# Performance work log

Hardware: AMD Instinct MI355X
Metric: run time of the kernel (lower is better)

## Reference

```python
import jax, jax.numpy as jnp
import numpy as np

N = 100000   # nodes
E = 625000   # edges
D = 128      # feature dim (layers = [128,128,128])
H = 8        # attention heads
HD = 16      # head dim (H*HD == D)


def setup_inputs() -> dict:
    key = jax.random.key(0)
    ks = jax.random.split(key, 16)
    s = 1.0 / np.sqrt(D).astype(np.float32)
    inp = {
        'x': jax.random.normal(ks[0], (N, D), dtype=jnp.float32),
        'edge_index': jax.random.randint(ks[1], (2, E), 0, N, dtype=jnp.int64),
        'W1': jax.random.normal(ks[2], (D, D), dtype=jnp.float32) * s,
        'b1': jnp.zeros((D,), jnp.float32),
        'W2': jax.random.normal(ks[3], (D, D), dtype=jnp.float32) * s,
        'b2': jnp.zeros((D,), jnp.float32),
        'Wq': jax.random.normal(ks[4], (D, H * HD), dtype=jnp.float32) * s,
        'bq': jnp.zeros((H * HD,), jnp.float32),
        'Wk': jax.random.normal(ks[5], (D, H * HD), dtype=jnp.float32) * s,
        'bk': jnp.zeros((H * HD,), jnp.float32),
        'Wv': jax.random.normal(ks[6], (D, H * HD), dtype=jnp.float32) * s,
        'bv': jnp.zeros((H * HD,), jnp.float32),
        'Wo': jax.random.normal(ks[7], (H * HD, D), dtype=jnp.float32) * s,
        'bo': jnp.zeros((D,), jnp.float32),
    }
    return inp


def _gcn_conv(x, W, b, src, dst):
    """PyG GCNConv: x' = D^-1/2 (A+I) D^-1/2 (x W) + b, symmetric norm with self-loops."""
    h = x @ W                                   # [N, Dout]
    # degree at targets, +1 for self-loop
    deg = jnp.ones((N,), h.dtype).at[dst].add(jnp.ones((E,), h.dtype))
    dinv = jax.lax.rsqrt(deg)                   # [N]
    norm = dinv[src] * dinv[dst]                # [E]
    agg = jnp.zeros_like(h).at[dst].add(h[src] * norm[:, None])
    agg = agg + h * (dinv * dinv)[:, None]      # self-loop term
    return agg + b


def _mha_seq1(x, Wq, bq, Wk, bk, Wv, bv, Wo, bo):
    """Faithful to the hand-rolled MHA: batch=N, implied seq_len=1."""
    n = x.shape[0]
    q = (x @ Wq + bq).reshape(n, 1, H, HD).transpose(0, 2, 1, 3)  # [N,H,1,HD]
    k = (x @ Wk + bk).reshape(n, 1, H, HD).transpose(0, 2, 1, 3)
    v = (x @ Wv + bv).reshape(n, 1, H, HD).transpose(0, 2, 1, 3)
    scores = jnp.einsum('nhqd,nhkd->nhqk', q, k) / np.float32(np.sqrt(HD))
    attn = jax.nn.softmax(scores, axis=-1)                        # [N,H,1,1]
    out = jnp.einsum('nhqk,nhkd->nhqd', attn, v)                  # [N,H,1,HD]
    out = out.transpose(0, 2, 1, 3).reshape(n, 1, H * HD)
    return out @ Wo + bo                                          # [N,1,D]


def reference(x, edge_index, W1, b1, W2, b2, Wq, bq, Wk, bk, Wv, bv, Wo, bo):
    src, dst = edge_index[0], edge_index[1]
    h = _gcn_conv(x, W1, b1, src, dst)
    h = jax.nn.relu(h)                 # dropout is identity in eval
    h = _gcn_conv(h, W2, b2, src, dst) # last conv: no relu
    return _mha_seq1(h, Wq, bq, Wk, bk, Wv, bv, Wo, bo)
```

## Files before the change

kernel.cpp:

```cpp
#include <hip/hip_runtime.h>
#include <hip/hip_bf16.h>

#define DD 128
#define CAP 16
#define OVF_MAX 8192
#define ECHUNK 2048

typedef __bf16 bf16x8v __attribute__((ext_vector_type(8)));
typedef float  f32x4   __attribute__((ext_vector_type(4)));

__device__ inline unsigned short f2bf(float f) {
    unsigned u = __builtin_bit_cast(unsigned, f);
    unsigned r = (u + 0x7fffu + ((u >> 16) & 1u)) >> 16;
    return (unsigned short)r;
}
__device__ inline float bflo2f(unsigned p) { return __builtin_bit_cast(float, p << 16); }
__device__ inline float bfhi2f(unsigned p) { return __builtin_bit_cast(float, p & 0xffff0000u); }
__device__ inline float rl_f(int v, int i) {
    return __builtin_bit_cast(float, __builtin_amdgcn_readlane(v, i));
}

__global__ __launch_bounds__(256) void k_zero(int* __restrict__ a, int N) {
    int i = blockIdx.x * 256 + threadIdx.x;
    int stride = gridDim.x * 256;
    for (; i <= N; i += stride) a[i] = 0;
}

__global__ __launch_bounds__(256) void k_fill_fuse1(const int* __restrict__ src, const int* __restrict__ dst,
                                                    int* __restrict__ fillc, int* __restrict__ srcp,
                                                    int* __restrict__ ovfcnt, int2* __restrict__ ovf,
                                                    int E, int N, int FB,
                                                    const float* __restrict__ Wv, const float* __restrict__ Wo,
                                                    const float* __restrict__ bv, const float* __restrict__ bo,
                                                    float* __restrict__ Wf, float* __restrict__ bfo) {
    if ((int)blockIdx.x < FB) {
        int bin   = blockIdx.x & 7;
        int chunk = blockIdx.x >> 3;
        int binsz = (N + 7) / 8;
        int lo = bin * binsz;
        int hi = lo + binsz; if (hi > N) hi = N;
        int base = chunk * ECHUNK + threadIdx.x;
        #pragma unroll
        for (int i = 0; i < ECHUNK / 256; ++i) {
            int e = base + i * 256;
            if (e < E) {
                int d = dst[e];
                if (d >= lo && d < hi) {
                    int s = src[e];
                    if ((unsigned)s < (unsigned)N) {
                        int pos = atomicAdd(&fillc[d], 1);
                        if (pos < CAP) srcp[(size_t)d * CAP + pos] = s;
                        else {
                            int op = atomicAdd(ovfcnt, 1);
                            if (op < OVF_MAX) ovf[op] = make_int2(s, d);
                        }
                    }
                }
            }
        }
    } else {
        int gid = (blockIdx.x - FB) * 256 + threadIdx.x;
        if (gid >= (DD + 1) * DD) return;
        int i = gid >> 7, j = gid & (DD - 1);
        if (i < DD) {
            float acc = 0.f;
            for (int k = 0; k < DD; ++k) acc = fmaf(Wv[i * DD + k], Wo[k * DD + j], acc);
            Wf[i * DD + j] = acc;
        } else {
            float acc = bo[j];
            for (int k = 0; k < DD; ++k) acc = fmaf(bv[k], Wo[k * DD + j], acc);
            bfo[j] = acc;
        }
    }
}

__global__ __launch_bounds__(256) void k_dinv_wprep(const int* __restrict__ fillc, float* __restrict__ dinv,
                                                    int N, int nb,
                                                    const float* __restrict__ W2, const float* __restrict__ Wf,
                                                    const float* __restrict__ b2, const float* __restrict__ bfo,
                                                    unsigned short* __restrict__ W2ft, float* __restrict__ bf2,
                                                    const float* __restrict__ W1, unsigned short* __restrict__ Wt1) {
    if ((int)blockIdx.x < nb) {
        int n = blockIdx.x * 256 + threadIdx.x;
        if (n < N) dinv[n] = rsqrtf(1.0f + (float)fillc[n]);
    } else {
        int blk = blockIdx.x - nb;
        if (blk < 65) {
            int gid = blk * 256 + threadIdx.x;
            if (gid >= (DD + 1) * DD) return;
            int i = gid >> 7, j = gid & (DD - 1);
            if (i < DD) {
                float acc = 0.f;
                for (int k = 0; k < DD; ++k) acc = fmaf(W2[i * DD + k], Wf[k * DD + j], acc);
                W2ft[j * DD + i] = f2bf(acc);
            } else {
                float acc = bfo[j];
                for (int k = 0; k < DD; ++k) acc = fmaf(b2[k], Wf[k * DD + j], acc);
                bf2[j] = acc;
            }
        } else {
            int gid = (blk - 65) * 256 + threadIdx.x;
            int k = gid >> 7, n = gid & 127;
            Wt1[n * DD + k] = f2bf(W1[k * DD + n]);
        }
    }
}

__global__ __launch_bounds__(256, 2) void k_gemm_mfma(const float* __restrict__ Af,
                                                      const unsigned short* __restrict__ Wt,
                                                      unsigned short* __restrict__ Cb, int M) {
    int w  = threadIdx.x >> 6;
    int l  = threadIdx.x & 63;
    int lr = l & 15, lg = l >> 4;

    bf16x8v bfr[8][4];
    #pragma unroll
    for (int nt = 0; nt < 8; ++nt)
        #pragma unroll
        for (int kk = 0; kk < 4; ++kk)
            bfr[nt][kk] = *reinterpret_cast<const bf16x8v*>(Wt + (nt * 16 + lr) * DD + kk * 32 + lg * 8);

    int tiles = (M + 63) >> 6;
    for (int t = blockIdx.x; t < tiles; t += gridDim.x) {
        int m0 = t * 64 + w * 16;
        int row = m0 + lr;
        int rowc = row < M ? row : (M - 1);

        bf16x8v af[4];
        #pragma unroll
        for (int kk = 0; kk < 4; ++kk) {
            const float* p = Af + (size_t)rowc * DD + kk * 32 + lg * 8;
            float4 u0 = *reinterpret_cast<const float4*>(p);
            float4 u1 = *reinterpret_cast<const float4*>(p + 4);
            af[kk][0] = (__bf16)u0.x; af[kk][1] = (__bf16)u0.y;
            af[kk][2] = (__bf16)u0.z; af[kk][3] = (__bf16)u0.w;
            af[kk][4] = (__bf16)u1.x; af[kk][5] = (__bf16)u1.y;
            af[kk][6] = (__bf16)u1.z; af[kk][7] = (__bf16)u1.w;
        }

        f32x4 acc[8] = {};
        #pragma unroll
        for (int kk = 0; kk < 4; ++kk)
            #pragma unroll
            for (int nt = 0; nt < 8; ++nt)
                acc[nt] = __builtin_amdgcn_mfma_f32_16x16x32_bf16(af[kk], bfr[nt][kk], acc[nt], 0, 0, 0);

        #pragma unroll
        for (int nt = 0; nt < 8; ++nt)
            #pragma unroll
            for (int r = 0; r < 4; ++r) {
                int rr = m0 + lg * 4 + r;
                if (rr < M) Cb[(size_t)rr * DD + nt * 16 + lr] = f2bf(acc[nt][r]);
            }
    }
}

__global__ __launch_bounds__(256) void k_gg(const int* __restrict__ fillc, const int* __restrict__ srcp,
                                            const float* __restrict__ dinv, const unsigned* __restrict__ h32,
                                            const float* __restrict__ b1, const unsigned short* __restrict__ W2ft,
                                            unsigned short* __restrict__ hA2, int N,
                                            const int* __restrict__ ovfcnt, const int2* __restrict__ ovf) {
    __shared__ unsigned short Wl[128][136];
    __shared__ unsigned short agg[16][136];
    int t = threadIdx.x;
    {
        const unsigned* Wsrc = (const unsigned*)W2ft;
        #pragma unroll
        for (int i = 0; i < 32; ++i) {
            int idx = t + i * 256;
            int row = idx >> 6, col = idx & 63;
            *reinterpret_cast<unsigned*>(&Wl[row][col * 2]) = Wsrc[idx];
        }
    }
    int l = t & 63;
    int w = t >> 6;
    int m0 = blockIdx.x * 16 + w * 4;

    float2 bb = reinterpret_cast<const float2*>(b1)[l];
    int fcidx = m0 + l; if (fcidx >= N) fcidx = N - 1;
    int fc = (l < 4) ? fillc[fcidx] : 0;

    int deg[4], c[4], sv[4], wvb[4];
    #pragma unroll
    for (int r = 0; r < 4; ++r) {
        deg[r] = __builtin_amdgcn_readlane(fc, r);
        int cc = deg[r] > CAP ? CAP : deg[r];
        c[r] = cc;
        int row = (m0 + r < N) ? (m0 + r) : (N - 1);
        sv[r] = (cc > 0) ? srcp[(size_t)row * CAP + (l < cc ? l : cc - 1)] : 0;
    }
    #pragma unroll
    for (int r = 0; r < 4; ++r)
        wvb[r] = __builtin_bit_cast(int, dinv[sv[r]]);

    unsigned p[4][8]; float wgt[4][8];
    #pragma unroll
    for (int r = 0; r < 4; ++r) {
        int f = c[r] < 8 ? c[r] : 8;
        #pragma unroll
        for (int q = 0; q < 8; ++q) {
            int i = (q < f) ? q : (f > 0 ? f - 1 : 0);
            int s = __builtin_amdgcn_readlane(sv[r], i);
            p[r][q] = h32[(size_t)s * 64 + l];
            wgt[r][q] = (q < f) ? rl_f(wvb[r], i) : 0.f;
        }
    }
    unsigned ps[4];
    #pragma unroll
    for (int r = 0; r < 4; ++r) {
        int n = m0 + r; int nc = n < N ? n : N - 1;
        ps[r] = h32[(size_t)nc * 64 + l];
    }

    float ax[4] = {0.f, 0.f, 0.f, 0.f}, ay[4] = {0.f, 0.f, 0.f, 0.f};
    #pragma unroll
    for (int r = 0; r < 4; ++r)
        #pragma unroll
        for (int q = 0; q < 8; ++q) {
            ax[r] = fmaf(wgt[r][q], bflo2f(p[r][q]), ax[r]);
            ay[r] = fmaf(wgt[r][q], bfhi2f(p[r][q]), ay[r]);
        }
    #pragma unroll
    for (int r = 0; r < 4; ++r) {
        for (int i = 8; i < c[r]; i += 8) {
            #pragma unroll
            for (int q = 0; q < 8; ++q) {
                int ii = (i + q < c[r]) ? i + q : c[r] - 1;
                int s = __builtin_amdgcn_readlane(sv[r], ii);
                unsigned pp = h32[(size_t)s * 64 + l];
                float wq = (i + q < c[r]) ? rl_f(wvb[r], ii) : 0.f;
                ax[r] = fmaf(wq, bflo2f(pp), ax[r]);
                ay[r] = fmaf(wq, bfhi2f(pp), ay[r]);
            }
        }
    }
    int anyovf = 0;
    #pragma unroll
    for (int r = 0; r < 4; ++r) anyovf |= (deg[r] > CAP) ? 1 : 0;
    if (anyovf) {
        int oc = *ovfcnt; if (oc > OVF_MAX) oc = OVF_MAX;
        for (int i = 0; i < oc; ++i) {
            int2 e = ovf[i];
            #pragma unroll
            for (int r = 0; r < 4; ++r) {
                if (deg[r] > CAP && e.y == m0 + r) {
                    float wq = dinv[e.x];
                    unsigned pp = h32[(size_t)e.x * 64 + l];
                    ax[r] = fmaf(wq, bflo2f(pp), ax[r]);
                    ay[r] = fmaf(wq, bfhi2f(pp), ay[r]);
                }
            }
        }
    }
    #pragma unroll
    for (int r = 0; r < 4; ++r) {
        int n = m0 + r;
        float di = rsqrtf(1.0f + (float)deg[r]);
        float di2 = di * di;
        float ox = fmaf(di2, bflo2f(ps[r]), di * ax[r]) + bb.x;
        float oy = fmaf(di2, bfhi2f(ps[r]), di * ay[r]) + bb.y;
        ox = fmaxf(ox, 0.f); oy = fmaxf(oy, 0.f);
        unsigned po = (n < N) ? ((unsigned)f2bf(ox) | ((unsigned)f2bf(oy) << 16)) : 0u;
        *reinterpret_cast<unsigned*>(&agg[w * 4 + r][l * 2]) = po;
    }
    __syncthreads();

    int lr = l & 15, lg = l >> 4;
    f32x4 acc[2] = {};
    #pragma unroll
    for (int kk = 0; kk < 4; ++kk) {
        bf16x8v af = *reinterpret_cast<const bf16x8v*>(&agg[lr][kk * 32 + lg * 8]);
        #pragma unroll
        for (int j = 0; j < 2; ++j) {
            int nt = w * 2 + j;
            bf16x8v bfrag = *reinterpret_cast<const bf16x8v*>(&Wl[nt * 16 + lr][kk * 32 + lg * 8]);
            acc[j] = __builtin_amdgcn_mfma_f32_16x16x32_bf16(af, bfrag, acc[j], 0, 0, 0);
        }
    }
    int mb = blockIdx.x * 16;
    #pragma unroll
    for (int j = 0; j < 2; ++j) {
        int nt = w * 2 + j;
        #pragma unroll
        for (int r4 = 0; r4 < 4; ++r4) {
            int rr = mb + lg * 4 + r4;
            if (rr < N) hA2[(size_t)rr * DD + nt * 16 + lr] = f2bf(acc[j][r4]);
        }
    }
}

__global__ __launch_bounds__(256) void k_gather_pad(const int* __restrict__ fillc, const int* __restrict__ srcp,
                                                    const float* __restrict__ dinv, const unsigned* __restrict__ h32,
                                                    const float* __restrict__ bias, float* __restrict__ outp,
                                                    int N, const int* __restrict__ ovfcnt, const int2* __restrict__ ovf) {
    int l = threadIdx.x & 63;
    int g = blockIdx.x * 4 + (threadIdx.x >> 6);
    int m0 = g * 4;
    if (m0 >= N) return;
    float2 bb = reinterpret_cast<const float2*>(bias)[l];

    int fcidx = m0 + l; if (fcidx >= N) fcidx = N - 1;
    int fc = (l < 4) ? fillc[fcidx] : 0;

    int deg[4], c[4], sv[4], wvb[4];
    #pragma unroll
    for (int r = 0; r < 4; ++r) {
        deg[r] = __builtin_amdgcn_readlane(fc, r);
        int cc = deg[r] > CAP ? CAP : deg[r];
        c[r] = cc;
        int row = (m0 + r < N) ? (m0 + r) : (N - 1);
        sv[r] = (cc > 0) ? srcp[(size_t)row * CAP + (l < cc ? l : cc - 1)] : 0;
    }
    #pragma unroll
    for (int r = 0; r < 4; ++r)
        wvb[r] = __builtin_bit_cast(int, dinv[sv[r]]);

    unsigned p[4][8]; float w[4][8];
    #pragma unroll
    for (int r = 0; r < 4; ++r) {
        int f = c[r] < 8 ? c[r] : 8;
        #pragma unroll
        for (int q = 0; q < 8; ++q) {
            int i = (q < f) ? q : (f > 0 ? f - 1 : 0);
            int s = __builtin_amdgcn_readlane(sv[r], i);
            p[r][q] = h32[(size_t)s * 64 + l];
            w[r][q] = (q < f) ? rl_f(wvb[r], i) : 0.f;
        }
    }
    unsigned ps[4];
    #pragma unroll
    for (int r = 0; r < 4; ++r) {
        int n = m0 + r; int nc = n < N ? n : N - 1;
        ps[r] = h32[(size_t)nc * 64 + l];
    }

    float ax[4] = {0.f, 0.f, 0.f, 0.f}, ay[4] = {0.f, 0.f, 0.f, 0.f};
    #pragma unroll
    for (int r = 0; r < 4; ++r)
        #pragma unroll
        for (int q = 0; q < 8; ++q) {
            ax[r] = fmaf(w[r][q], bflo2f(p[r][q]), ax[r]);
            ay[r] = fmaf(w[r][q], bfhi2f(p[r][q]), ay[r]);
        }
    #pragma unroll
    for (int r = 0; r < 4; ++r) {
        for (int i = 8; i < c[r]; i += 8) {
            #pragma unroll
            for (int q = 0; q < 8; ++q) {
                int ii = (i + q < c[r]) ? i + q : c[r] - 1;
                int s = __builtin_amdgcn_readlane(sv[r], ii);
                unsigned pp = h32[(size_t)s * 64 + l];
                float wq = (i + q < c[r]) ? rl_f(wvb[r], ii) : 0.f;
                ax[r] = fmaf(wq, bflo2f(pp), ax[r]);
                ay[r] = fmaf(wq, bfhi2f(pp), ay[r]);
            }
        }
    }
    int anyovf = 0;
    #pragma unroll
    for (int r = 0; r < 4; ++r) anyovf |= (deg[r] > CAP) ? 1 : 0;
    if (anyovf) {
        int oc = *ovfcnt; if (oc > OVF_MAX) oc = OVF_MAX;
        for (int i = 0; i < oc; ++i) {
            int2 e = ovf[i];
            #pragma unroll
            for (int r = 0; r < 4; ++r) {
                if (deg[r] > CAP && e.y == m0 + r) {
                    float wq = dinv[e.x];
                    unsigned pp = h32[(size_t)e.x * 64 + l];
                    ax[r] = fmaf(wq, bflo2f(pp), ax[r]);
                    ay[r] = fmaf(wq, bfhi2f(pp), ay[r]);
                }
            }
        }
    }
    #pragma unroll
    for (int r = 0; r < 4; ++r) {
        int n = m0 + r;
        if (n < N) {
            float di = rsqrtf(1.0f + (float)deg[r]);
            float di2 = di * di;
            float ox = fmaf(di2, bflo2f(ps[r]), di * ax[r]) + bb.x;
            float oy = fmaf(di2, bfhi2f(ps[r]), di * ay[r]) + bb.y;
            reinterpret_cast<float2*>(outp)[(size_t)n * 64 + l] = make_float2(ox, oy);
        }
    }
}

extern "C" void kernel_launch(void* const* d_in, const int* in_sizes, int n_in,
                              void* d_out, int out_size, void* d_ws, size_t ws_size,
                              hipStream_t stream) {
    const float* x  = (const float*)d_in[0];
    const int*   ei = (const int*)d_in[1];
    const float* W1 = (const float*)d_in[2];
    const float* b1 = (const float*)d_in[3];
    const float* W2 = (const float*)d_in[4];
    const float* b2 = (const float*)d_in[5];
    const float* Wv = (const float*)d_in[10];
    const float* bv = (const float*)d_in[11];
    const float* Wo = (const float*)d_in[12];
    const float* bo = (const float*)d_in[13];
    int N = in_sizes[0] / DD;
    int E = in_sizes[1] / 2;
    const int* src = ei;
    const int* dst = ei + E;
    float* out = (float*)d_out;

    unsigned* hA  = (unsigned*)d_ws;
    unsigned* hA2 = hA + (size_t)N * 64;
    float* dinv   = (float*)(hA2 + (size_t)N * 64);
    float* Wf     = dinv + N;
    float* bfo    = Wf + DD * DD;
    float* bf2    = bfo + DD;
    unsigned short* Wt1  = (unsigned short*)(bf2 + DD);
    unsigned short* W2ft = Wt1 + DD * DD;
    int* fillc  = (int*)(W2ft + DD * DD);
    int* ovfcnt = fillc + N;
    int2* ovf   = (int2*)(((uintptr_t)(ovfcnt + 1) + 63) & ~(uintptr_t)63);
    int* srcp   = (int*)(((uintptr_t)(ovf + OVF_MAX) + 63) & ~(uintptr_t)63);

    int nb = (N + 255) / 256;
    int nchunks = (E + ECHUNK - 1) / ECHUNK;
    int FB = nchunks * 8;

    k_zero<<<512, 256, 0, stream>>>(fillc, N);
    k_fill_fuse1<<<FB + 129, 256, 0, stream>>>(src, dst, fillc, srcp, ovfcnt, ovf, E, N, FB,
                                               Wv, Wo, bv, bo, Wf, bfo);
    k_dinv_wprep<<<nb + 129, 256, 0, stream>>>(fillc, dinv, N, nb,
                                               W2, Wf, b2, bfo, W2ft, bf2, W1, Wt1);
    k_gemm_mfma<<<512, 256, 0, stream>>>(x, Wt1, (unsigned short*)hA, N);
    int ggb = (N + 15) / 16;
    k_gg<<<ggb, 256, 0, stream>>>(fillc, srcp, dinv, hA, b1, W2ft, (unsigned short*)hA2, N, ovfcnt, ovf);
    int gb = ((N + 3) / 4 + 3) / 4;
    k_gather_pad<<<gb, 256, 0, stream>>>(fillc, srcp, dinv, hA2, bf2, out, N, ovfcnt, ovf);
}
```

Before: 161.8 us.

## Drop dinv kernel by recomputing rsqrt from degree counts and regroup prep kernels

Removes the separate dinv pass by computing rsqrt(1+deg) inline in both gather kernels from the fill counts. The zero-fill, Wv·Wo fusion and W1 transpose now share one prep kernel, and the W2·Wf fold moves into the edge-fill kernel. This cuts the launch count from six to five, at the cost of an extra rsqrt per gathered neighbour.

Measured after the change: 157.1 us. -2.9%, faster.

```diff
diff --git a/kernel.cpp b/kernel.cpp
--- a/kernel.cpp
+++ b/kernel.cpp
@@ -20,19 +20,43 @@
     return __builtin_bit_cast(float, __builtin_amdgcn_readlane(v, i));
 }
 
-__global__ __launch_bounds__(256) void k_zero(int* __restrict__ a, int N) {
-    int i = blockIdx.x * 256 + threadIdx.x;
-    int stride = gridDim.x * 256;
-    for (; i <= N; i += stride) a[i] = 0;
-}
-
-__global__ __launch_bounds__(256) void k_fill_fuse1(const int* __restrict__ src, const int* __restrict__ dst,
+__global__ __launch_bounds__(256) void k_prep1(int* __restrict__ fillc, int N, int ZB,
+                                               const float* __restrict__ Wv, const float* __restrict__ Wo,
+                                               const float* __restrict__ bv, const float* __restrict__ bo,
+                                               float* __restrict__ Wf, float* __restrict__ bfo,
+                                               const float* __restrict__ W1, unsigned short* __restrict__ Wt1) {
+    int blk = blockIdx.x;
+    if (blk < ZB) {
+        int i = blk * 256 + threadIdx.x;
+        int stride = ZB * 256;
+        for (; i <= N; i += stride) fillc[i] = 0;
+    } else if (blk < ZB + 65) {
+        int gid = (blk - ZB) * 256 + threadIdx.x;
+        if (gid >= (DD + 1) * DD) return;
+        int i = gid >> 7, j = gid & (DD - 1);
+        if (i < DD) {
+            float acc = 0.f;
+            for (int k = 0; k < DD; ++k) acc = fmaf(Wv[i * DD + k], Wo[k * DD + j], acc);
+            Wf[i * DD + j] = acc;
+        } else {
+            float acc = bo[j];
+            for (int k = 0; k < DD; ++k) acc = fmaf(bv[k], Wo[k * DD + j], acc);
+            bfo[j] = acc;
+        }
+    } else {
+        int gid = (blk - ZB - 65) * 256 + threadIdx.x;
+        int k = gid >> 7, n = gid & 127;
+        Wt1[n * DD + k] = f2bf(W1[k * DD + n]);
+    }
+}
+
+__global__ __launch_bounds__(256) void k_fill_wprep(const int* __restrict__ src, const int* __restrict__ dst,
                                                     int* __restrict__ fillc, int* __restrict__ srcp,
                                                     int* __restrict__ ovfcnt, int2* __restrict__ ovf,
                                                     int E, int N, int FB,
-                                                    const float* __restrict__ Wv, const float* __restrict__ Wo,
-                                                    const float* __restrict__ bv, const float* __restrict__ bo,
-                                                    float* __restrict__ Wf, float* __restrict__ bfo) {
+                                                    const float* __restrict__ W2, const float* __restrict__ Wf,
+                                                    const float* __restrict__ b2, const float* __restrict__ bfo,
+                                                    unsigned short* __restrict__ W2ft, float* __restrict__ bf2) {
     if ((int)blockIdx.x < FB) {
         int bin   = blockIdx.x & 7;
         int chunk = blockIdx.x >> 3;
@@ -64,44 +88,12 @@
         int i = gid >> 7, j = gid & (DD - 1);
         if (i < DD) {
             float acc = 0.f;
-            for (int k = 0; k < DD; ++k) acc = fmaf(Wv[i * DD + k], Wo[k * DD + j], acc);
-            Wf[i * DD + j] = acc;
+            for (int k = 0; k < DD; ++k) acc = fmaf(W2[i * DD + k], Wf[k * DD + j], acc);
+            W2ft[j * DD + i] = f2bf(acc);
         } else {
-            float acc = bo[j];
-            for (int k = 0; k < DD; ++k) acc = fmaf(bv[k], Wo[k * DD + j], acc);
-            bfo[j] = acc;
-        }
-    }
-}
-
-__global__ __launch_bounds__(256) void k_dinv_wprep(const int* __restrict__ fillc, float* __restrict__ dinv,
-                                                    int N, int nb,
-                                                    const float* __restrict__ W2, const float* __restrict__ Wf,
-                                                    const float* __restrict__ b2, const float* __restrict__ bfo,
-                                                    unsigned short* __restrict__ W2ft, float* __restrict__ bf2,
-                                                    const float* __restrict__ W1, unsigned short* __restrict__ Wt1) {
-    if ((int)blockIdx.x < nb) {
-        int n = blockIdx.x * 256 + threadIdx.x;
-        if (n < N) dinv[n] = rsqrtf(1.0f + (float)fillc[n]);
-    } else {
-        int blk = blockIdx.x - nb;
-        if (blk < 65) {
-            int gid = blk * 256 + threadIdx.x;
-            if (gid >= (DD + 1) * DD) return;
-            int i = gid >> 7, j = gid & (DD - 1);
-            if (i < DD) {
-                float acc = 0.f;
-                for (int k = 0; k < DD; ++k) acc = fmaf(W2[i * DD + k], Wf[k * DD + j], acc);
-                W2ft[j * DD + i] = f2bf(acc);
-            } else {
-                float acc = bfo[j];
-                for (int k = 0; k < DD; ++k) acc = fmaf(b2[k], Wf[k * DD + j], acc);
-                bf2[j] = acc;
-            }
-        } else {
-            int gid = (blk - 65) * 256 + threadIdx.x;
-            int k = gid >> 7, n = gid & 127;
-            Wt1[n * DD + k] = f2bf(W1[k * DD + n]);
+            float acc = bfo[j];
+            for (int k = 0; k < DD; ++k) acc = fmaf(b2[k], Wf[k * DD + j], acc);
+            bf2[j] = acc;
         }
     }
 }
@@ -156,7 +148,7 @@
 }
 
 __global__ __launch_bounds__(256) void k_gg(const int* __restrict__ fillc, const int* __restrict__ srcp,
-                                            const float* __restrict__ dinv, const unsigned* __restrict__ h32,
+                                            const unsigned* __restrict__ h32,
                                             const float* __restrict__ b1, const unsigned short* __restrict__ W2ft,
                                             unsigned short* __restrict__ hA2, int N,
                                             const int* __restrict__ ovfcnt, const int2* __restrict__ ovf) {
@@ -191,7 +183,7 @@
     }
     #pragma unroll
     for (int r = 0; r < 4; ++r)
-        wvb[r] = __builtin_bit_cast(int, dinv[sv[r]]);
+        wvb[r] = __builtin_bit_cast(int, rsqrtf(1.0f + (float)fillc[sv[r]]));
 
     unsigned p[4][8]; float wgt[4][8];
     #pragma unroll
@@ -244,7 +236,7 @@
             #pragma unroll
             for (int r = 0; r < 4; ++r) {
                 if (deg[r] > CAP && e.y == m0 + r) {
-                    float wq = dinv[e.x];
+                    float wq = rsqrtf(1.0f + (float)fillc[e.x]);
                     unsigned pp = h32[(size_t)e.x * 64 + l];
                     ax[r] = fmaf(wq, bflo2f(pp), ax[r]);
                     ay[r] = fmaf(wq, bfhi2f(pp), ay[r]);
@@ -290,7 +282,7 @@
 }
 
 __global__ __launch_bounds__(256) void k_gather_pad(const int* __restrict__ fillc, const int* __restrict__ srcp,
-                                                    const float* __restrict__ dinv, const unsigned* __restrict__ h32,
+                                                    const unsigned* __restrict__ h32,
                                                     const float* __restrict__ bias, float* __restrict__ outp,
                                                     int N, const int* __restrict__ ovfcnt, const int2* __restrict__ ovf) {
     int l = threadIdx.x & 63;
@@ -313,7 +305,7 @@
     }
     #pragma unroll
     for (int r = 0; r < 4; ++r)
-        wvb[r] = __builtin_bit_cast(int, dinv[sv[r]]);
+        wvb[r] = __builtin_bit_cast(int, rsqrtf(1.0f + (float)fillc[sv[r]]));
 
     unsigned p[4][8]; float w[4][8];
     #pragma unroll
@@ -366,7 +358,7 @@
             #pragma unroll
             for (int r = 0; r < 4; ++r) {
                 if (deg[r] > CAP && e.y == m0 + r) {
-                    float wq = dinv[e.x];
+                    float wq = rsqrtf(1.0f + (float)fillc[e.x]);
                     unsigned pp = h32[(size_t)e.x * 64 + l];
                     ax[r] = fmaf(wq, bflo2f(pp), ax[r]);
                     ay[r] = fmaf(wq, bfhi2f(pp), ay[r]);
@@ -408,8 +400,7 @@
 
     unsigned* hA  = (unsigned*)d_ws;
     unsigned* hA2 = hA + (size_t)N * 64;
-    float* dinv   = (float*)(hA2 + (size_t)N * 64);
-    float* Wf     = dinv + N;
+    float* Wf     = (float*)(hA2 + (size_t)N * 64);
     float* bfo    = Wf + DD * DD;
     float* bf2    = bfo + DD;
     unsigned short* Wt1  = (unsigned short*)(bf2 + DD);
@@ -419,18 +410,16 @@
     int2* ovf   = (int2*)(((uintptr_t)(ovfcnt + 1) + 63) & ~(uintptr_t)63);
     int* srcp   = (int*)(((uintptr_t)(ovf + OVF_MAX) + 63) & ~(uintptr_t)63);
 
-    int nb = (N + 255) / 256;
     int nchunks = (E + ECHUNK - 1) / ECHUNK;
     int FB = nchunks * 8;
-
-    k_zero<<<512, 256, 0, stream>>>(fillc, N);
-    k_fill_fuse1<<<FB + 129, 256, 0, stream>>>(src, dst, fillc, srcp, ovfcnt, ovf, E, N, FB,
-                                               Wv, Wo, bv, bo, Wf, bfo);
-    k_dinv_wprep<<<nb + 129, 256, 0, stream>>>(fillc, dinv, N, nb,
-                                               W2, Wf, b2, bfo, W2ft, bf2, W1, Wt1);
+    int ZB = 512;
+
+    k_prep1<<<ZB + 65 + 64, 256, 0, stream>>>(fillc, N, ZB, Wv, Wo, bv, bo, Wf, bfo, W1, Wt1);
+    k_fill_wprep<<<FB + 65, 256, 0, stream>>>(src, dst, fillc, srcp, ovfcnt, ovf, E, N, FB,
+                                              W2, Wf, b2, bfo, W2ft, bf2);
     k_gemm_mfma<<<512, 256, 0, stream>>>(x, Wt1, (unsigned short*)hA, N);
     int ggb = (N + 15) / 16;
-    k_gg<<<ggb, 256, 0, stream>>>(fillc, srcp, dinv, hA, b1, W2ft, (unsigned short*)hA2, N, ovfcnt, ovf);
+    k_gg<<<ggb, 256, 0, stream>>>(fillc, srcp, hA, b1, W2ft, (unsigned short*)hA2, N, ovfcnt, ovf);
     int gb = ((N + 3) / 4 + 3) / 4;
-    k_gather_pad<<<gb, 256, 0, stream>>>(fillc, srcp, dinv, hA2, bf2, out, N, ovfcnt, ovf);
-}
+    k_gather_pad<<<gb, 256, 0, stream>>>(fillc, srcp, hA2, bf2, out, N, ovfcnt, ovf);
+}
```
